# Performance work log

Hardware: AMD Instinct MI355X
Metric: run time of the kernel (lower is better)

The kernel has to match this reference:

```python
import jax, jax.numpy as jnp
import numpy as np
from jax.scipy.stats import norm as jnorm

B, S, D, H, E, K, FF = 8, 256, 1024, 16, 4, 2, 4096
HD = D // H
NOISE_EPS = 0.01
LOSS_COEF = 0.01
EPS_FILL = float(np.finfo(float).eps)


def _ln(x, g, b):
    m = x.mean(-1, keepdims=True)
    v = x.var(-1, keepdims=True)
    return (x - m) * jax.lax.rsqrt(v + 1e-5) * g + b


def setup_inputs() -> dict:
    key = jax.random.key(0)
    ks = jax.random.split(key, 16)
    r = lambda i, shape, s=1.0: jax.random.normal(ks[i], shape, dtype=jnp.float32) * s
    return {
        "x": r(0, (B, S, D)),
        "e_outputs": r(1, (B, 64, D)),            # unused (is_lm=True) but part of signature
        "noise": r(2, (B, E)),                     # the randn_like(clean_logits) draw
        "w_gate": r(3, (D, E), 0.02),
        "w_noise": r(4, (D, E), 0.02),
        "Wq": r(5, (E, D, D), 0.02),
        "Wk": r(6, (E, D, D), 0.02),
        "Wv": r(7, (E, D, D), 0.02),
        "Wo": r(8, (E, D, D), 0.02),
        "W1": r(9, (E, D, FF), 0.02),
        "b1": jnp.zeros((E, FF), jnp.float32),
        "W2": r(10, (E, FF, D), 0.02),
        "b2": jnp.zeros((E, D), jnp.float32),
        "g1": jnp.ones((E, D), jnp.float32),
        "be1": jnp.zeros((E, D), jnp.float32),
        "g2": jnp.ones((E, D), jnp.float32),
        "be2": jnp.zeros((E, D), jnp.float32),
        "trg_mask": jnp.tril(jnp.ones((S, S), dtype=bool))[None, None],  # causal [1,1,S,S]
        "src_mask": jnp.ones((1, 1, 1, 64), dtype=bool),                 # unused (is_lm=True)
    }


def _cv_squared(v):
    # torch .var() is unbiased (ddof=1)
    return v.var(ddof=1) / (v.mean() ** 2 + 1e-10)


def reference(x, e_outputs, noise, w_gate, w_noise, Wq, Wk, Wv, Wo, W1, b1, W2, b2,
              g1, be1, g2, be2, trg_mask, src_mask):
    b, s, d = x.shape
    # ---- noisy top-k gating (per sample, on the sequence-sum) ----
    xs = x.sum(axis=1)                                   # [B, D]
    clean = xs @ w_gate                                  # [B, E]
    raw_noise = xs @ w_noise                             # [B, E]
    stddev = jax.nn.softplus(raw_noise) + NOISE_EPS      # train=True -> *1.0
    noisy = clean + noise * stddev                       # logits
    top_logits, top_idx = jax.lax.top_k(noisy, K + 1)    # [B, K+1]
    topk_gates = jax.nn.softmax(top_logits[:, :K], axis=1)
    gates = jnp.zeros_like(noisy).at[jnp.arange(b)[:, None], top_idx[:, :K]].set(topk_gates)
    # load: prob each expert's clean logit lands in the noisy top-k
    thr_in = top_logits[:, K:K + 1]                      # (k+1)-th noisy value
    thr_out = top_logits[:, K - 1:K]                     # k-th noisy value
    is_in = noisy > thr_in
    prob = jnp.where(is_in,
                     jnorm.cdf((clean - thr_in) / stddev),
                     jnorm.cdf((clean - thr_out) / stddev))
    load = prob.sum(0)                                   # [E]
    importance = gates.sum(0)                            # [E]
    loss = (_cv_squared(importance) + _cv_squared(load)) * LOSS_COEF

    # ---- experts: standard decoder layer (self-attn + FFN), is_lm -> no cross-attn ----
    neg = jnp.asarray(-1e9, x.dtype)
    scale = 1.0 / np.sqrt(HD)

    def expert(p):
        wq, wk, wv, wo, w1, bb1, w2, bb2, gg1, bbe1, gg2, bbe2 = p
        q = (x @ wq).reshape(b, s, H, HD)
        k_ = (x @ wk).reshape(b, s, H, HD)
        v = (x @ wv).reshape(b, s, H, HD)
        scores = jnp.einsum('bqhd,bkhd->bhqk', q, k_) * scale
        scores = jnp.where(trg_mask, scores, neg)
        attn = jax.nn.softmax(scores, axis=-1)
        o = jnp.einsum('bhqk,bkhd->bqhd', attn, v).reshape(b, s, d) @ wo
        h = _ln(x + o, gg1, bbe1)
        ff = jax.nn.relu(h @ w1 + bb1) @ w2 + bb2
        return _ln(h + ff, gg2, bbe2)

    outs = jax.vmap(expert)((Wq, Wk, Wv, Wo, W1, b1, W2, b2, g1, be1, g2, be2))  # [E,B,S,D]

    # ---- combine: scatter-add of gate-weighted expert outputs (dense equivalent) ----
    y = jnp.einsum('be,ebsd->bsd', gates, outs)
    y = jnp.where(y == 0, jnp.asarray(EPS_FILL, y.dtype), y)
    return y, loss
```

## Files before the change

kernel.cpp:

```cpp
#include <hip/hip_runtime.h>
#include <hip/hip_bf16.h>

typedef __bf16 bf16;
typedef __attribute__((ext_vector_type(4))) __bf16 bf16x4;
typedef __attribute__((ext_vector_type(8))) __bf16 bf16x8;
typedef __attribute__((ext_vector_type(4))) float floatx4;

constexpr int CB = 8, CS = 256, CD = 1024, CH = 16, CE = 4, CFF = 4096, CHD = 64;
constexpr long long DD  = 1048576;
constexpr long long DFF = 4194304;
constexpr long long BSD = 2097152;
constexpr long long PSD = 4194304;

constexpr size_t OFF_PART = 0;
constexpr size_t OFF_CLEAN= 262144;
constexpr size_t OFF_RAW  = 262272;
constexpr size_t OFF_GATES= 262400;
constexpr size_t OFF_EACT = 262528;
constexpr size_t OFF_PBE  = 262592;
constexpr size_t OFF_BP   = 262656;
constexpr size_t OFF_XBF  = 263168;
constexpr size_t OFF_WT   = OFF_XBF + (size_t)BSD*2;
constexpr size_t OFF_W1T  = OFF_WT  + (size_t)16*DD*2;
constexpr size_t OFF_W2T  = OFF_W1T + (size_t)4*DFF*2;
constexpr size_t OFF_QKV  = OFF_W2T + (size_t)4*DFF*2;
constexpr size_t OFF_AO   = OFF_QKV + (size_t)3*PSD*2;
constexpr size_t OFF_F1   = OFF_QKV;
constexpr size_t OFF_PB   = OFF_AO  + (size_t)PSD*2;
constexpr size_t OFF_VT   = OFF_PB;
constexpr size_t OFF_H    = OFF_PB  + (size_t)2*PSD*4;
constexpr size_t OFF_HBF  = OFF_H   + (size_t)PSD*4;

__global__ __launch_bounds__(256)
void cvt_xsum(const float* __restrict__ x, bf16* __restrict__ xbf, float* __restrict__ part) {
  int blk = blockIdx.x;
  int b = blk >> 3, ch = blk & 7;
  int t = threadIdx.x;
  float s0 = 0.f, s1 = 0.f, s2 = 0.f, s3 = 0.f;
  long long base4 = ((long long)(b*CS + ch*32))*CD / 4;
#pragma unroll 4
  for (int r = 0; r < 32; ++r) {
    long long i4 = base4 + (long long)r*(CD/4) + t;
    float4 v = ((const float4*)x)[i4];
    bf16x4 o; o[0] = (bf16)v.x; o[1] = (bf16)v.y; o[2] = (bf16)v.z; o[3] = (bf16)v.w;
    ((bf16x4*)xbf)[i4] = o;
    s0 += v.x; s1 += v.y; s2 += v.z; s3 += v.w;
  }
  float4 sv; sv.x = s0; sv.y = s1; sv.z = s2; sv.w = s3;
  ((float4*)(part + (long long)blk*CD))[t] = sv;
}

__global__ __launch_bounds__(256)
void gate_dots(const float* __restrict__ part, const float* __restrict__ wg,
               const float* __restrict__ wn, float* __restrict__ clean, float* __restrict__ raw) {
  int p = blockIdx.x, b = p >> 2, e = p & 3;
  int t = threadIdx.x;
  float s1 = 0.f, s2 = 0.f;
  for (int d = t; d < CD; d += 256) {
    float xv = 0.f;
#pragma unroll
    for (int c = 0; c < 8; ++c) xv += part[(long long)(b*8 + c)*CD + d];
    s1 += xv * wg[d*CE + e];
    s2 += xv * wn[d*CE + e];
  }
  for (int off = 32; off; off >>= 1) { s1 += __shfl_xor(s1, off); s2 += __shfl_xor(s2, off); }
  __shared__ float r1[4], r2[4];
  int lane = t & 63, w = t >> 6;
  if (lane == 0) { r1[w] = s1; r2[w] = s2; }
  __syncthreads();
  if (t == 0) { clean[p] = r1[0]+r1[1]+r1[2]+r1[3]; raw[p] = r2[0]+r2[1]+r2[2]+r2[3]; }
}

__global__ void gating_kernel(const float* __restrict__ clean, const float* __restrict__ raw,
                              const float* __restrict__ noise, float* __restrict__ gates,
                              int* __restrict__ eact, int* __restrict__ pairBE,
                              int* __restrict__ batchPair, float* __restrict__ loss_out) {
  if (threadIdx.x != 0) return;
  float imp[CE] = {0,0,0,0}, load[CE] = {0,0,0,0};
  int act[CE] = {0,0,0,0};
  for (int b = 0; b < CB; ++b) {
    float cl[CE], sd[CE], ny[CE];
    for (int e = 0; e < CE; ++e) {
      cl[e] = clean[b*CE + e];
      float rw = raw[b*CE + e];
      float sp = fmaxf(rw, 0.f) + log1pf(expf(-fabsf(rw)));
      sd[e] = sp + 0.01f;
      ny[e] = cl[e] + noise[b*CE + e]*sd[e];
    }
    int idx[CE] = {0,1,2,3};
    for (int a = 0; a < 3; ++a) {
      int best = a;
      for (int c = a + 1; c < 4; ++c) if (ny[idx[c]] > ny[idx[best]]) best = c;
      int tt = idx[a]; idx[a] = idx[best]; idx[best] = tt;
    }
    float l0 = ny[idx[0]], l1 = ny[idx[1]], l2 = ny[idx[2]];
    float e1 = expf(l1 - l0);
    float g0 = 1.f/(1.f + e1), g1v = e1/(1.f + e1);
    for (int e = 0; e < CE; ++e) gates[b*CE + e] = 0.f;
    gates[b*CE + idx[0]] = g0; gates[b*CE + idx[1]] = g1v;
    imp[idx[0]] += g0; imp[idx[1]] += g1v;
    act[idx[0]] = 1; act[idx[1]] = 1;
    for (int e = 0; e < CE; ++e) {
      bool is_in = ny[e] > l2;
      float thr = is_in ? l2 : l1;
      float zz = (cl[e] - thr) / sd[e];
      load[e] += 0.5f * erfcf(-zz * 0.70710678118654752440f);
    }
  }
  int pe2p[CB][CE];
  int pc = 0;
  for (int e = 0; e < CE; ++e)
    for (int b = 0; b < CB; ++b)
      if (gates[b*CE + e] != 0.f) { pairBE[pc] = b | (e << 8); pe2p[b][e] = pc; ++pc; }
  for (int b = 0; b < CB; ++b) {
    int s = 0;
    for (int e = 0; e < CE; ++e)
      if (gates[b*CE + e] != 0.f) batchPair[2*b + (s++)] = pe2p[b][e];
  }
  float m1 = 0.f, m2 = 0.f;
  for (int e = 0; e < CE; ++e) { m1 += imp[e]; m2 += load[e]; }
  m1 *= 0.25f; m2 *= 0.25f;
  float v1 = 0.f, v2 = 0.f;
  for (int e = 0; e < CE; ++e) { float d1 = imp[e]-m1, d2 = load[e]-m2; v1 += d1*d1; v2 += d2*d2; }
  v1 *= (1.f/3.f); v2 *= (1.f/3.f);
  loss_out[0] = 0.01f * (v1/(m1*m1 + 1e-10f) + v2/(m2*m2 + 1e-10f));
  for (int e = 0; e < CE; ++e) eact[e] = act[e];
}

__global__ __launch_bounds__(256)
void wtrans_reg(const float* __restrict__ Wq, const float* __restrict__ Wk,
                const float* __restrict__ Wv, const float* __restrict__ Wo,
                const float* __restrict__ W1, const float* __restrict__ W2,
                bf16* __restrict__ wT, bf16* __restrict__ w1T, bf16* __restrict__ w2T,
                const int* __restrict__ eact) {
  int zb = blockIdx.x;
  int w = threadIdx.x >> 6;
  const float* src; bf16* d; int rows, cols, btk, btn, e;
  if (zb < 1024) {
    int m = zb >> 6, bt = zb & 63; e = m >> 2; int which = m & 3;
    src = ((which == 0) ? Wq : (which == 1) ? Wk : (which == 2) ? Wv : Wo) + (long long)e*DD;
    d = wT + (long long)m*DD; rows = 1024; cols = 1024;
    btk = bt >> 3; btn = bt & 7;
  } else if (zb < 2048) {
    int z2 = zb - 1024; e = z2 >> 8; int bt = z2 & 255;
    src = W1 + (long long)e*DFF; d = w1T + (long long)e*DFF;
    rows = 1024; cols = 4096; btk = bt >> 5; btn = bt & 31;
  } else {
    int z3 = zb - 2048; e = z3 >> 8; int bt = z3 & 255;
    src = W2 + (long long)e*DFF; d = w2T + (long long)e*DFF;
    rows = 4096; cols = 1024; btk = bt >> 3; btn = bt & 7;
  }
  if (eact[e] == 0) return;
  int tk = btk*2 + (w & 1);
  int tn = btn*2 + (w >> 1);
  int lane = threadIdx.x & 63;
  int ln = lane >> 3, lk = lane & 7;
  int k0 = tk*64, n0 = tn*64;
  const float* s = src + (long long)(k0 + lk*8)*cols + n0 + ln*8;
  float4 f[8][2];
#pragma unroll
  for (int j = 0; j < 8; ++j) {
    f[j][0] = *(const float4*)(s + (long long)j*cols);
    f[j][1] = *(const float4*)(s + (long long)j*cols + 4);
  }
  bf16* dp = d + (long long)(n0 + ln*8)*rows + k0 + lk*8;
#pragma unroll
  for (int jn = 0; jn < 8; ++jn) {
    bf16x8 o;
#pragma unroll
    for (int jk = 0; jk < 8; ++jk) {
      const float* fp = (const float*)&f[jk][jn >> 2];
      o[jk] = (bf16)fp[jn & 3];
    }
    *(bf16x8*)(dp + (long long)jn*rows) = o;
  }
}

__global__ __launch_bounds__(256)
void transpose_v(const bf16* __restrict__ qkvC, bf16* __restrict__ vTb) {
  int z = blockIdx.z; int p = z >> 4, h = z & 15;
  const bf16* v = qkvC + 2*PSD + (long long)(p*CS)*CD + h*CHD;
  bf16* vt = vTb + (long long)(p*CH + h)*CHD*CS;
  __shared__ bf16 tile[32][33];
  int s0 = blockIdx.x*32, d0 = blockIdx.y*32;
  int tx = threadIdx.x % 32, ty = threadIdx.x / 32;
#pragma unroll
  for (int i = 0; i < 4; ++i)
    tile[ty + 8*i][tx] = v[(long long)(s0 + ty + 8*i)*CD + d0 + tx];
  __syncthreads();
#pragma unroll
  for (int i = 0; i < 4; ++i)
    vt[(long long)(d0 + ty + 8*i)*CS + s0 + tx] = tile[tx][ty + 8*i];
}

__device__ __forceinline__ void cp16(const bf16* g, bf16* l) {
  __builtin_amdgcn_global_load_lds((const __attribute__((address_space(1))) void*)g,
                                   (__attribute__((address_space(3))) void*)l, 16, 0, 0);
}

template<int R, int W>
__device__ __forceinline__ void stage(const bf16* __restrict__ src, int ld, bf16* dst) {
  constexpr int W8 = W/8;
  int t = threadIdx.x;
  int l = t & 63, wid = t >> 6;
#pragma unroll
  for (int i = 0; i < (R*W8)/256; ++i) {
    int idb = i*256 + wid*64;
    int id = idb + l;
    int row = id / W8, sl = id % W8;
    int gc = sl ^ (row & 7);
    cp16(src + (long long)row*ld + gc*8, dst + (long long)idb*8);
  }
}

__global__ __launch_bounds__(256)
void attn_fused(const bf16* __restrict__ qkvC, const bf16* __restrict__ vTb,
                bf16* __restrict__ aoC) {
  int h = blockIdx.x, p = blockIdx.y, qt = blockIdx.z;
  const bf16* qp = qkvC + (long long)(p*CS)*CD + h*CHD;
  const bf16* kp = qp + PSD;
  const bf16* vt = vTb + (long long)(p*CH + h)*CHD*CS;
  bf16* aop = aoC + (long long)(p*CS)*CD + h*CHD;

  __shared__ bf16 Ps[64*264];
  __shared__ float smaxL[64*4], ssumL[64*4], Lrow[64];

  int t = threadIdx.x, w = t >> 6, lane = t & 63, lr = lane & 15, quad = lane >> 4;

  floatx4 accs[4][4] = {};
  if (w <= qt) {
#pragma unroll
    for (int kk = 0; kk < 2; ++kk) {
      int c = kk*4 + quad;
      bf16x8 af[4], bfr[4];
#pragma unroll
      for (int i = 0; i < 4; ++i) {
        af[i]  = *(const bf16x8*)(qp + (long long)(qt*64 + i*16 + lr)*CD + c*8);
        bfr[i] = *(const bf16x8*)(kp + (long long)(w*64  + i*16 + lr)*CD + c*8);
      }
#pragma unroll
      for (int i = 0; i < 4; ++i)
#pragma unroll
        for (int j = 0; j < 4; ++j)
          accs[i][j] = __builtin_amdgcn_mfma_f32_16x16x32_bf16(af[i], bfr[j], accs[i][j], 0, 0, 0);
    }
  }
  float rmax[4][4];
#pragma unroll
  for (int i = 0; i < 4; ++i)
#pragma unroll
    for (int r = 0; r < 4; ++r) {
      int qrow = qt*64 + i*16 + quad*4 + r;
      float m = -3.0e38f;
#pragma unroll
      for (int j = 0; j < 4; ++j) {
        int kcol = w*64 + j*16 + lr;
        float s = accs[i][j][r]*0.125f;
        s = (kcol <= qrow) ? s : -3.0e38f;
        accs[i][j][r] = s;
        m = fmaxf(m, s);
      }
      rmax[i][r] = m;
    }
#pragma unroll
  for (int off = 1; off <= 8; off <<= 1)
#pragma unroll
    for (int i = 0; i < 4; ++i)
#pragma unroll
      for (int r = 0; r < 4; ++r) rmax[i][r] = fmaxf(rmax[i][r], __shfl_xor(rmax[i][r], off));
  if (lr == 0)
#pragma unroll
    for (int i = 0; i < 4; ++i)
#pragma unroll
      for (int r = 0; r < 4; ++r) smaxL[(i*16 + quad*4 + r)*4 + w] = rmax[i][r];
  __syncthreads();
  float rsum[4][4];
#pragma unroll
  for (int i = 0; i < 4; ++i)
#pragma unroll
    for (int r = 0; r < 4; ++r) {
      floatx4 mv = *(const floatx4*)&smaxL[(i*16 + quad*4 + r)*4];
      float M = fmaxf(fmaxf(mv[0], mv[1]), fmaxf(mv[2], mv[3]));
      float srow = 0.f;
#pragma unroll
      for (int j = 0; j < 4; ++j) {
        float pp = __expf(accs[i][j][r] - M);
        accs[i][j][r] = pp;
        srow += pp;
      }
      rsum[i][r] = srow;
    }
#pragma unroll
  for (int off = 1; off <= 8; off <<= 1)
#pragma unroll
    for (int i = 0; i < 4; ++i)
#pragma unroll
      for (int r = 0; r < 4; ++r) rsum[i][r] += __shfl_xor(rsum[i][r], off);
  if (lr == 0)
#pragma unroll
    for (int i = 0; i < 4; ++i)
#pragma unroll
      for (int r = 0; r < 4; ++r) ssumL[(i*16 + quad*4 + r)*4 + w] = rsum[i][r];
  __syncthreads();
  if (w == 0 && lr == 0) {
#pragma unroll
    for (int i = 0; i < 4; ++i)
#pragma unroll
      for (int r = 0; r < 4; ++r) {
        int m = i*16 + quad*4 + r;
        floatx4 sv = *(const floatx4*)&ssumL[m*4];
        Lrow[m] = sv[0] + sv[1] + sv[2] + sv[3];
      }
  }
  if (w <= qt) {
#pragma unroll
    for (int i = 0; i < 4; ++i)
#pragma unroll
      for (int j = 0; j < 4; ++j)
#pragma unroll
        for (int r = 0; r < 4; ++r)
          Ps[(i*16 + quad*4 + r)*264 + w*64 + j*16 + lr] = (bf16)accs[i][j][r];
  }
  __syncthreads();
  floatx4 acco[4] = {};
  int ksMax = (qt + 1)*2;
  for (int ks = 0; ks < ksMax; ++ks) {
    int c = ks*4 + quad;
    bf16x8 ap = *(const bf16x8*)(Ps + (w*16 + lr)*264 + c*8);
#pragma unroll
    for (int j = 0; j < 4; ++j) {
      bf16x8 bv = *(const bf16x8*)(vt + (long long)(j*16 + lr)*CS + c*8);
      acco[j] = __builtin_amdgcn_mfma_f32_16x16x32_bf16(ap, bv, acco[j], 0, 0, 0);
    }
  }
#pragma unroll
  for (int r = 0; r < 4; ++r) {
    int orow = w*16 + quad*4 + r;
    float inv = 1.f / Lrow[orow];
#pragma unroll
    for (int j = 0; j < 4; ++j)
      aop[(long long)(qt*64 + orow)*CD + j*16 + lr] = (bf16)(acco[j][r]*inv);
  }
}

__global__ __launch_bounds__(256)
void ln1_kernel(const float* __restrict__ x, const float* __restrict__ PbF,
                const float* __restrict__ gamma, const float* __restrict__ beta,
                float* __restrict__ h, bf16* __restrict__ hbf, const int* __restrict__ pairBE) {
  int row = blockIdx.x;
  int pbe = pairBE[row >> 8]; int pb = pbe & 255, pe = pbe >> 8;
  int t = threadIdx.x;
  float4 a = ((const float4*)(x + ((long long)pb*CS + (row & 255))*CD))[t];
  float4 b = ((const float4*)(PbF + (long long)row*CD))[t];
  float4 c = ((const float4*)(PbF + PSD + (long long)row*CD))[t];
  float v0 = a.x + b.x + c.x, v1 = a.y + b.y + c.y;
  float v2 = a.z + b.z + c.z, v3 = a.w + b.w + c.w;
  float s  = v0 + v1 + v2 + v3;
  float s2 = v0*v0 + v1*v1 + v2*v2 + v3*v3;
  int lane = t & 63, wave = t >> 6;
  for (int off = 32; off; off >>= 1) { s += __shfl_xor(s, off); s2 += __shfl_xor(s2, off); }
  __shared__ float red[8];
  if (lane == 0) { red[wave*2] = s; red[wave*2 + 1] = s2; }
  __syncthreads();
  s  = red[0] + red[2] + red[4] + red[6];
  s2 = red[1] + red[3] + red[5] + red[7];
  float mean = s * (1.f/CD);
  float rstd = rsqrtf(s2*(1.f/CD) - mean*mean + 1e-5f);
  float4 gm = ((const float4*)(gamma + (long long)pe*CD))[t];
  float4 bt = ((const float4*)(beta  + (long long)pe*CD))[t];
  float4 o;
  o.x = (v0 - mean)*rstd*gm.x + bt.x;
  o.y = (v1 - mean)*rstd*gm.y + bt.y;
  o.z = (v2 - mean)*rstd*gm.z + bt.z;
  o.w = (v3 - mean)*rstd*gm.w + bt.w;
  ((float4*)(h + (long long)row*CD))[t] = o;
  bf16x4 ob; ob[0] = (bf16)o.x; ob[1] = (bf16)o.y; ob[2] = (bf16)o.z; ob[3] = (bf16)o.w;
  ((bf16x4*)(hbf + (long long)row*CD))[t] = ob;
}

__global__ __launch_bounds__(256)
void ln2y_kernel(const float* __restrict__ h, const bf16* __restrict__ PbB,
                 const float* __restrict__ gamma, const float* __restrict__ beta,
                 float* __restrict__ y, const float* __restrict__ gates,
                 const int* __restrict__ pairBE, const int* __restrict__ batchPair) {
  int row = blockIdx.x;
  int b = row >> 8, sIdx = row & 255;
  int p0 = batchPair[2*b], p1 = batchPair[2*b + 1];
  int e0 = pairBE[p0] >> 8, e1 = pairBE[p1] >> 8;
  float gv0 = gates[b*CE + e0], gv1 = gates[b*CE + e1];
  long long r0 = (long long)p0*CS + sIdx, r1 = (long long)p1*CS + sIdx;
  int t = threadIdx.x;
  float4 a = ((const float4*)(h + r0*CD))[t];
  float4 c = ((const float4*)(h + r1*CD))[t];
#pragma unroll
  for (int k = 0; k < 4; ++k) {
    bf16x4 pa = ((const bf16x4*)(PbB + (long long)k*PSD + r0*CD))[t];
    bf16x4 pc = ((const bf16x4*)(PbB + (long long)k*PSD + r1*CD))[t];
    a.x += (float)pa[0]; a.y += (float)pa[1]; a.z += (float)pa[2]; a.w += (float)pa[3];
    c.x += (float)pc[0]; c.y += (float)pc[1]; c.z += (float)pc[2]; c.w += (float)pc[3];
  }
  float sA = a.x + a.y + a.z + a.w;
  float sA2 = a.x*a.x + a.y*a.y + a.z*a.z + a.w*a.w;
  float sB = c.x + c.y + c.z + c.w;
  float sB2 = c.x*c.x + c.y*c.y + c.z*c.z + c.w*c.w;
  int lane = t & 63, wave = t >> 6;
  for (int off = 32; off; off >>= 1) {
    sA += __shfl_xor(sA, off); sA2 += __shfl_xor(sA2, off);
    sB += __shfl_xor(sB, off); sB2 += __shfl_xor(sB2, off);
  }
  __shared__ float red[16];
  if (lane == 0) { red[wave*4] = sA; red[wave*4+1] = sA2; red[wave*4+2] = sB; red[wave*4+3] = sB2; }
  __syncthreads();
  sA  = red[0] + red[4] + red[8]  + red[12];
  sA2 = red[1] + red[5] + red[9]  + red[13];
  sB  = red[2] + red[6] + red[10] + red[14];
  sB2 = red[3] + red[7] + red[11] + red[15];
  float mA = sA*(1.f/CD), mB = sB*(1.f/CD);
  float rsA = rsqrtf(sA2*(1.f/CD) - mA*mA + 1e-5f);
  float rsB = rsqrtf(sB2*(1.f/CD) - mB*mB + 1e-5f);
  float4 gm0 = ((const float4*)(gamma + (long long)e0*CD))[t];
  float4 bt0 = ((const float4*)(beta  + (long long)e0*CD))[t];
  float4 gm1 = ((const float4*)(gamma + (long long)e1*CD))[t];
  float4 bt1 = ((const float4*)(beta  + (long long)e1*CD))[t];
  float4 o;
  o.x = gv0*((a.x - mA)*rsA*gm0.x + bt0.x) + gv1*((c.x - mB)*rsB*gm1.x + bt1.x);
  o.y = gv0*((a.y - mA)*rsA*gm0.y + bt0.y) + gv1*((c.y - mB)*rsB*gm1.y + bt1.y);
  o.z = gv0*((a.z - mA)*rsA*gm0.z + bt0.z) + gv1*((c.z - mB)*rsB*gm1.z + bt1.z);
  o.w = gv0*((a.w - mA)*rsA*gm0.w + bt0.w) + gv1*((c.w - mB)*rsB*gm1.w + bt1.w);
  constexpr float EF = 2.2204460492503131e-16f;
  o.x = (o.x == 0.f) ? EF : o.x;  o.y = (o.y == 0.f) ? EF : o.y;
  o.z = (o.z == 0.f) ? EF : o.z;  o.w = (o.w == 0.f) ? EF : o.w;
  ((float4*)(y + (long long)row*CD))[t] = o;
}

enum { EPI_BF16 = 0, EPI_F32 = 1, EPI_BRELU = 2, EPI_BIASBF16 = 3 };

template<int EPI, int KS, bool A_BATCH>
__global__ __launch_bounds__(256)
void gemm_nt(const bf16* __restrict__ A, const bf16* __restrict__ Bt, void* __restrict__ Cv,
             int K , int lda, int ldb, int ldc,
             long long oBe, long long oBmat, long long oCmat, long long oCk,
             const float* __restrict__ bias, long long biasStride,
             const int* __restrict__ pairBE) {
  constexpr int BM = 128, BN = 128;
  int z = blockIdx.z;
  int zk = z % KS, mat = z / KS;
  int gx = gridDim.x;
  int nwg = gx * gridDim.y;
  int lin = blockIdx.x + gx*blockIdx.y;
  int nl  = (lin & 7)*(nwg >> 3) + (lin >> 3);
  int m0 = (nl % gx) * BM, n0 = (nl / gx) * BN;
  int pbe = pairBE[m0 >> 8]; int pb = pbe & 255, pe = pbe >> 8;
  const bf16* Ab = A + (A_BATCH ? ((long long)pb*CS + (m0 & 255))*lda : (long long)m0*lda)
                     + (long long)zk*K;
  const bf16* Bb = Bt + (long long)pe*oBe + (long long)mat*oBmat + (long long)zk*K
                      + (long long)n0*ldb;
  long long coff = (long long)mat*oCmat + (long long)zk*oCk;

  __shared__ bf16 As[BM*64];
  __shared__ bf16 Bs[BN*64];

  int wave = threadIdx.x >> 6;
  int lane = threadIdx.x & 63;
  int wm = wave >> 1, wn = wave & 1;
  int lr = lane & 15;
  int quad = lane >> 4;

  floatx4 acc[4][4] = {};

  for (int kt = 0; kt < K; kt += 64) {
    stage<BM, 64>(Ab + kt, lda, As);
    stage<BN, 64>(Bb + kt, ldb, Bs);
    __syncthreads();
#pragma unroll
    for (int kk = 0; kk < 2; ++kk) {
      bf16x8 af[4], bfr[4];
#pragma unroll
      for (int i = 0; i < 4; ++i) {
        int c = kk*4 + quad;
        int m = wm*64 + i*16 + lr;
        af[i]  = *(const bf16x8*)(As + m*64 + ((c ^ (m & 7))*8));
        int n = wn*64 + i*16 + lr;
        bfr[i] = *(const bf16x8*)(Bs + n*64 + ((c ^ (n & 7))*8));
      }
#pragma unroll
      for (int i = 0; i < 4; ++i)
#pragma unroll
        for (int j = 0; j < 4; ++j)
          acc[i][j] = __builtin_amdgcn_mfma_f32_16x16x32_bf16(af[i], bfr[j], acc[i][j], 0, 0, 0);
    }
    __syncthreads();
  }

#pragma unroll
  for (int j = 0; j < 4; ++j) {
    int col = n0 + wn*64 + j*16 + lr;
    float bv = 0.f;
    if constexpr (EPI == EPI_BRELU || EPI == EPI_BIASBF16)
      if (zk == 0) bv = bias[(long long)pe*biasStride + col];
#pragma unroll
    for (int i = 0; i < 4; ++i) {
#pragma unroll
      for (int r = 0; r < 4; ++r) {
        int row = m0 + wm*64 + i*16 + quad*4 + r;
        float v = acc[i][j][r] + bv;
        long long idx = coff + (long long)row*ldc + col;
        if constexpr (EPI == EPI_BF16)          ((bf16*)Cv)[idx] = (bf16)v;
        else if constexpr (EPI == EPI_F32)      ((float*)Cv)[idx] = v;
        else if constexpr (EPI == EPI_BRELU)    ((bf16*)Cv)[idx] = (bf16)fmaxf(v, 0.f);
        else                                    ((bf16*)Cv)[idx] = (bf16)v;
      }
    }
  }
}

extern "C" void kernel_launch(void* const* d_in, const int* in_sizes, int n_in,
                              void* d_out, int out_size, void* d_ws, size_t ws_size,
                              hipStream_t stream) {
  const float* x       = (const float*)d_in[0];
  const float* noise   = (const float*)d_in[2];
  const float* w_gate  = (const float*)d_in[3];
  const float* w_noise = (const float*)d_in[4];
  const float* Wq      = (const float*)d_in[5];
  const float* Wk      = (const float*)d_in[6];
  const float* Wv      = (const float*)d_in[7];
  const float* Wo      = (const float*)d_in[8];
  const float* W1      = (const float*)d_in[9];
  const float* b1      = (const float*)d_in[10];
  const float* W2      = (const float*)d_in[11];
  const float* b2      = (const float*)d_in[12];
  const float* g1      = (const float*)d_in[13];
  const float* be1     = (const float*)d_in[14];
  const float* g2      = (const float*)d_in[15];
  const float* be2     = (const float*)d_in[16];

  char* ws = (char*)d_ws;
  float* y    = (float*)d_out;
  float* loss = y + (size_t)BSD;

  float* part  = (float*)(ws + OFF_PART);
  float* clean = (float*)(ws + OFF_CLEAN);
  float* raw   = (float*)(ws + OFF_RAW);
  float* gates = (float*)(ws + OFF_GATES);
  int*   eact  = (int*)  (ws + OFF_EACT);
  int*   pairBE= (int*)  (ws + OFF_PBE);
  int*   batchPair = (int*)(ws + OFF_BP);
  bf16*  xbf   = (bf16*) (ws + OFF_XBF);
  bf16*  wT    = (bf16*) (ws + OFF_WT);
  bf16*  w1T   = (bf16*) (ws + OFF_W1T);
  bf16*  w2T   = (bf16*) (ws + OFF_W2T);
  bf16*  qkvC  = (bf16*) (ws + OFF_QKV);
  bf16*  aoC   = (bf16*) (ws + OFF_AO);
  bf16*  f1    = (bf16*) (ws + OFF_F1);
  bf16*  vTb   = (bf16*) (ws + OFF_VT);
  float* PbF   = (float*)(ws + OFF_PB);
  bf16*  PbB   = (bf16*) (ws + OFF_PB);
  float* h     = (float*)(ws + OFF_H);
  bf16*  hbf   = (bf16*) (ws + OFF_HBF);

  cvt_xsum<<<64, 256, 0, stream>>>(x, xbf, part);
  gate_dots<<<32, 256, 0, stream>>>(part, w_gate, w_noise, clean, raw);
  gating_kernel<<<1, 64, 0, stream>>>(clean, raw, noise, gates, eact, pairBE, batchPair, loss);
  wtrans_reg<<<3072, 256, 0, stream>>>(Wq, Wk, Wv, Wo, W1, W2, wT, w1T, w2T, eact);

  gemm_nt<EPI_BF16, 1, true><<<dim3(32, 8, 3), 256, 0, stream>>>(
      xbf, wT, qkvC, 1024, 1024, 1024, 1024,
      4*DD, DD, PSD, 0, nullptr, 0, pairBE);

  transpose_v<<<dim3(8, 2, 256), 256, 0, stream>>>(qkvC, vTb);

  attn_fused<<<dim3(CH, 16, 4), 256, 0, stream>>>(qkvC, vTb, aoC);

  gemm_nt<EPI_F32, 2, false><<<dim3(32, 8, 2), 256, 0, stream>>>(
      aoC, wT + 3*DD, PbF, 512, 1024, 1024, 1024,
      4*DD, 0, 0, PSD, nullptr, 0, pairBE);

  ln1_kernel<<<4096, 256, 0, stream>>>(x, PbF, g1, be1, h, hbf, pairBE);

  gemm_nt<EPI_BRELU, 1, false><<<dim3(32, 32, 1), 256, 0, stream>>>(
      hbf, w1T, f1, 1024, 1024, 1024, 4096,
      DFF, 0, 0, 0, b1, CFF, pairBE);

  gemm_nt<EPI_BIASBF16, 4, false><<<dim3(32, 8, 4), 256, 0, stream>>>(
      f1, w2T, PbB, 1024, 4096, 4096, 1024,
      DFF, 0, 0, PSD, b2, CD, pairBE);

  ln2y_kernel<<<2048, 256, 0, stream>>>(h, PbB, g2, be2, y, gates, pairBE, batchPair);
}
```

Before: 508.6 us.

## Fuse x conversion into weight transpose and register-transpose V

Merges the x bf16 conversion/partial-sum kernel into the weight transpose launch so both run concurrently, and moves the weight transpose before gating, which drops the inactive-expert skip. Uses nontemporal loads for weight reads. Rewrites the V transpose to use per-thread register 8x8 transposes with 16-byte accesses instead of an LDS tile. It risks converting weights of experts that gating would have skipped.

```diff
diff --git a/kernel.cpp b/kernel.cpp
--- a/kernel.cpp
+++ b/kernel.cpp
@@ -32,22 +32,68 @@
 constexpr size_t OFF_HBF  = OFF_H   + (size_t)PSD*4;
 
 __global__ __launch_bounds__(256)
-void cvt_xsum(const float* __restrict__ x, bf16* __restrict__ xbf, float* __restrict__ part) {
-  int blk = blockIdx.x;
-  int b = blk >> 3, ch = blk & 7;
-  int t = threadIdx.x;
-  float s0 = 0.f, s1 = 0.f, s2 = 0.f, s3 = 0.f;
-  long long base4 = ((long long)(b*CS + ch*32))*CD / 4;
+void wtrans_cvt(const float* __restrict__ Wq, const float* __restrict__ Wk,
+                const float* __restrict__ Wv, const float* __restrict__ Wo,
+                const float* __restrict__ W1, const float* __restrict__ W2,
+                bf16* __restrict__ wT, bf16* __restrict__ w1T, bf16* __restrict__ w2T,
+                const float* __restrict__ x, bf16* __restrict__ xbf, float* __restrict__ part) {
+  int zb = blockIdx.x;
+  if (zb >= 3072) {
+    int blk = zb - 3072;
+    int b = blk >> 3, ch = blk & 7;
+    int t = threadIdx.x;
+    float s0 = 0.f, s1 = 0.f, s2 = 0.f, s3 = 0.f;
+    long long base4 = ((long long)(b*CS + ch*32))*CD / 4;
 #pragma unroll 4
-  for (int r = 0; r < 32; ++r) {
-    long long i4 = base4 + (long long)r*(CD/4) + t;
-    float4 v = ((const float4*)x)[i4];
-    bf16x4 o; o[0] = (bf16)v.x; o[1] = (bf16)v.y; o[2] = (bf16)v.z; o[3] = (bf16)v.w;
-    ((bf16x4*)xbf)[i4] = o;
-    s0 += v.x; s1 += v.y; s2 += v.z; s3 += v.w;
-  }
-  float4 sv; sv.x = s0; sv.y = s1; sv.z = s2; sv.w = s3;
-  ((float4*)(part + (long long)blk*CD))[t] = sv;
+    for (int r = 0; r < 32; ++r) {
+      long long i4 = base4 + (long long)r*(CD/4) + t;
+      float4 v = ((const float4*)x)[i4];
+      bf16x4 o; o[0] = (bf16)v.x; o[1] = (bf16)v.y; o[2] = (bf16)v.z; o[3] = (bf16)v.w;
+      ((bf16x4*)xbf)[i4] = o;
+      s0 += v.x; s1 += v.y; s2 += v.z; s3 += v.w;
+    }
+    float4 sv; sv.x = s0; sv.y = s1; sv.z = s2; sv.w = s3;
+    ((float4*)(part + (long long)blk*CD))[t] = sv;
+    return;
+  }
+  int w = threadIdx.x >> 6;
+  const float* src; bf16* d; int rows, cols, btk, btn;
+  if (zb < 1024) {
+    int m = zb >> 6, bt = zb & 63; int e = m >> 2; int which = m & 3;
+    src = ((which == 0) ? Wq : (which == 1) ? Wk : (which == 2) ? Wv : Wo) + (long long)e*DD;
+    d = wT + (long long)m*DD; rows = 1024; cols = 1024;
+    btk = bt >> 3; btn = bt & 7;
+  } else if (zb < 2048) {
+    int z2 = zb - 1024; int e = z2 >> 8; int bt = z2 & 255;
+    src = W1 + (long long)e*DFF; d = w1T + (long long)e*DFF;
+    rows = 1024; cols = 4096; btk = bt >> 5; btn = bt & 31;
+  } else {
+    int z3 = zb - 2048; int e = z3 >> 8; int bt = z3 & 255;
+    src = W2 + (long long)e*DFF; d = w2T + (long long)e*DFF;
+    rows = 4096; cols = 1024; btk = bt >> 3; btn = bt & 7;
+  }
+  int tk = btk*2 + (w & 1);
+  int tn = btn*2 + (w >> 1);
+  int lane = threadIdx.x & 63;
+  int ln = lane >> 3, lk = lane & 7;
+  int k0 = tk*64, n0 = tn*64;
+  const float* s = src + (long long)(k0 + lk*8)*cols + n0 + ln*8;
+  floatx4 f[8][2];
+#pragma unroll
+  for (int j = 0; j < 8; ++j) {
+    f[j][0] = __builtin_nontemporal_load((const floatx4*)(s + (long long)j*cols));
+    f[j][1] = __builtin_nontemporal_load((const floatx4*)(s + (long long)j*cols + 4));
+  }
+  bf16* dp = d + (long long)(n0 + ln*8)*rows + k0 + lk*8;
+#pragma unroll
+  for (int jn = 0; jn < 8; ++jn) {
+    bf16x8 o;
+#pragma unroll
+    for (int jk = 0; jk < 8; ++jk) {
+      o[jk] = (bf16)f[jk][jn >> 2][jn & 3];
+    }
+    *(bf16x8*)(dp + (long long)jn*rows) = o;
+  }
 }
 
 __global__ __launch_bounds__(256)
@@ -128,69 +174,22 @@
 }
 
 __global__ __launch_bounds__(256)
-void wtrans_reg(const float* __restrict__ Wq, const float* __restrict__ Wk,
-                const float* __restrict__ Wv, const float* __restrict__ Wo,
-                const float* __restrict__ W1, const float* __restrict__ W2,
-                bf16* __restrict__ wT, bf16* __restrict__ w1T, bf16* __restrict__ w2T,
-                const int* __restrict__ eact) {
-  int zb = blockIdx.x;
-  int w = threadIdx.x >> 6;
-  const float* src; bf16* d; int rows, cols, btk, btn, e;
-  if (zb < 1024) {
-    int m = zb >> 6, bt = zb & 63; e = m >> 2; int which = m & 3;
-    src = ((which == 0) ? Wq : (which == 1) ? Wk : (which == 2) ? Wv : Wo) + (long long)e*DD;
-    d = wT + (long long)m*DD; rows = 1024; cols = 1024;
-    btk = bt >> 3; btn = bt & 7;
-  } else if (zb < 2048) {
-    int z2 = zb - 1024; e = z2 >> 8; int bt = z2 & 255;
-    src = W1 + (long long)e*DFF; d = w1T + (long long)e*DFF;
-    rows = 1024; cols = 4096; btk = bt >> 5; btn = bt & 31;
-  } else {
-    int z3 = zb - 2048; e = z3 >> 8; int bt = z3 & 255;
-    src = W2 + (long long)e*DFF; d = w2T + (long long)e*DFF;
-    rows = 4096; cols = 1024; btk = bt >> 3; btn = bt & 7;
-  }
-  if (eact[e] == 0) return;
-  int tk = btk*2 + (w & 1);
-  int tn = btn*2 + (w >> 1);
-  int lane = threadIdx.x & 63;
+void transpose_v(const bf16* __restrict__ qkvC, bf16* __restrict__ vTb) {
+  int z = blockIdx.x; int p = z >> 4, h = z & 15;
+  int w = threadIdx.x >> 6, lane = threadIdx.x & 63;
   int ln = lane >> 3, lk = lane & 7;
-  int k0 = tk*64, n0 = tn*64;
-  const float* s = src + (long long)(k0 + lk*8)*cols + n0 + ln*8;
-  float4 f[8][2];
-#pragma unroll
-  for (int j = 0; j < 8; ++j) {
-    f[j][0] = *(const float4*)(s + (long long)j*cols);
-    f[j][1] = *(const float4*)(s + (long long)j*cols + 4);
-  }
-  bf16* dp = d + (long long)(n0 + ln*8)*rows + k0 + lk*8;
-#pragma unroll
-  for (int jn = 0; jn < 8; ++jn) {
+  const bf16* v = qkvC + 2*PSD + ((long long)(p*CS + w*64 + ln*8))*CD + h*CHD + lk*8;
+  bf16x8 in[8];
+#pragma unroll
+  for (int j = 0; j < 8; ++j) in[j] = *(const bf16x8*)(v + (long long)j*CD);
+  bf16* vt = vTb + ((long long)(p*CH + h)*CHD + lk*8)*CS + w*64 + ln*8;
+#pragma unroll
+  for (int dn = 0; dn < 8; ++dn) {
     bf16x8 o;
 #pragma unroll
-    for (int jk = 0; jk < 8; ++jk) {
-      const float* fp = (const float*)&f[jk][jn >> 2];
-      o[jk] = (bf16)fp[jn & 3];
-    }
-    *(bf16x8*)(dp + (long long)jn*rows) = o;
-  }
-}
-
-__global__ __launch_bounds__(256)
-void transpose_v(const bf16* __restrict__ qkvC, bf16* __restrict__ vTb) {
-  int z = blockIdx.z; int p = z >> 4, h = z & 15;
-  const bf16* v = qkvC + 2*PSD + (long long)(p*CS)*CD + h*CHD;
-  bf16* vt = vTb + (long long)(p*CH + h)*CHD*CS;
-  __shared__ bf16 tile[32][33];
-  int s0 = blockIdx.x*32, d0 = blockIdx.y*32;
-  int tx = threadIdx.x % 32, ty = threadIdx.x / 32;
-#pragma unroll
-  for (int i = 0; i < 4; ++i)
-    tile[ty + 8*i][tx] = v[(long long)(s0 + ty + 8*i)*CD + d0 + tx];
-  __syncthreads();
-#pragma unroll
-  for (int i = 0; i < 4; ++i)
-    vt[(long long)(d0 + ty + 8*i)*CS + s0 + tx] = tile[tx][ty + 8*i];
+    for (int j = 0; j < 8; ++j) o[j] = in[j][dn];
+    *(bf16x8*)(vt + (long long)dn*CS) = o;
+  }
 }
 
 __device__ __forceinline__ void cp16(const bf16* g, bf16* l) {
@@ -558,16 +557,15 @@
   float* h     = (float*)(ws + OFF_H);
   bf16*  hbf   = (bf16*) (ws + OFF_HBF);
 
-  cvt_xsum<<<64, 256, 0, stream>>>(x, xbf, part);
+  wtrans_cvt<<<3136, 256, 0, stream>>>(Wq, Wk, Wv, Wo, W1, W2, wT, w1T, w2T, x, xbf, part);
   gate_dots<<<32, 256, 0, stream>>>(part, w_gate, w_noise, clean, raw);
   gating_kernel<<<1, 64, 0, stream>>>(clean, raw, noise, gates, eact, pairBE, batchPair, loss);
-  wtrans_reg<<<3072, 256, 0, stream>>>(Wq, Wk, Wv, Wo, W1, W2, wT, w1T, w2T, eact);
 
   gemm_nt<EPI_BF16, 1, true><<<dim3(32, 8, 3), 256, 0, stream>>>(
       xbf, wT, qkvC, 1024, 1024, 1024, 1024,
       4*DD, DD, PSD, 0, nullptr, 0, pairBE);
 
-  transpose_v<<<dim3(8, 2, 256), 256, 0, stream>>>(qkvC, vTb);
+  transpose_v<<<256, 256, 0, stream>>>(qkvC, vTb);
 
   attn_fused<<<dim3(CH, 16, 4), 256, 0, stream>>>(qkvC, vTb, aoC);
 
```

Measured after the change: 489.8 us. 1.04x faster.
